# Performance work log

Hardware: AMD Instinct MI355X
Metric: run time of the kernel (lower is better)

Reference implementation:

```python
import jax, jax.numpy as jnp
import numpy as np

E = 1024   # emb_dim
H = 1024   # hidden_size
L = 2      # num_layers
V = 50257  # vocab_size
S = 2048   # encoder input length
T = 2048   # decoder target length


def setup_inputs() -> dict:
    key = jax.random.key(0)
    ks = jax.random.split(key, 16)
    s = 0.02  # init scale
    f32 = jnp.float32
    return {
        "inputs": jax.random.randint(ks[0], (1, S), 0, V),
        "outputs": jax.random.randint(ks[1], (1, T), 0, V),
        "sos": 1,
        "enc_emb": jax.random.normal(ks[2], (V, E), f32) * s,
        "dec_emb": jax.random.normal(ks[3], (V, E), f32) * s,
        # Stacked LSTM weights; layer-0 input dim == E == H so layers stack.
        "enc_Wih": jax.random.normal(ks[4], (L, 4 * H, H), f32) * s,
        "enc_Whh": jax.random.normal(ks[5], (L, 4 * H, H), f32) * s,
        "enc_bih": jax.random.normal(ks[6], (L, 4 * H), f32) * s,
        "enc_bhh": jax.random.normal(ks[7], (L, 4 * H), f32) * s,
        "dec_Wih": jax.random.normal(ks[8], (L, 4 * H, H), f32) * s,
        "dec_Whh": jax.random.normal(ks[9], (L, 4 * H, H), f32) * s,
        "dec_bih": jax.random.normal(ks[10], (L, 4 * H), f32) * s,
        "dec_bhh": jax.random.normal(ks[11], (L, 4 * H), f32) * s,
        "lin_W": jax.random.normal(ks[12], (V, H), f32) * s,
        "lin_b": jax.random.normal(ks[13], (V,), f32) * s,
    }


def _run_stack(xs, Wih, Whh, bih, bhh, h0, c0):
    # xs: [S, E]; Wih/Whh: [L, 4H, H]; h0/c0: [L, H]
    # PyTorch LSTM gate order: i, f, g, o.
    h_fin, c_fin = [], []
    for l in range(Wih.shape[0]):
        Wi, Wh, bi, bh = Wih[l], Whh[l], bih[l], bhh[l]

        def step(carry, x, Wi=Wi, Wh=Wh, bi=bi, bh=bh):
            h, c = carry
            g = Wi @ x + bi + Wh @ h + bh           # [4H]
            i, f, gg, o = jnp.split(g, 4)
            c = jax.nn.sigmoid(f) * c + jax.nn.sigmoid(i) * jnp.tanh(gg)
            h = jax.nn.sigmoid(o) * jnp.tanh(c)
            return (h, c), h

        (h, c), xs = jax.lax.scan(step, (h0[l], c0[l]), xs)
        h_fin.append(h)
        c_fin.append(c)
    return xs, jnp.stack(h_fin), jnp.stack(c_fin)


def reference(inputs, outputs, sos, enc_emb, dec_emb,
              enc_Wih, enc_Whh, enc_bih, enc_bhh,
              dec_Wih, dec_Whh, dec_bih, dec_bhh,
              lin_W, lin_b):
    # Encoder over the source sequence (batch == 1, squeezed away).
    x = enc_emb[inputs[0]]                       # [S, E]
    z = jnp.zeros((L, H), dtype=x.dtype)
    _, hN, cN = _run_stack(x, enc_Wih, enc_Whh, enc_bih, enc_bhh, z, z)
    # Full teacher forcing: decoder inputs are [sos, outputs[:, :-1]].
    dec_tokens = jnp.concatenate(
        [jnp.array([sos], dtype=outputs.dtype), outputs[0, :-1]])
    y = dec_emb[dec_tokens]                      # [T, E]
    dec_out, _, _ = _run_stack(y, dec_Wih, dec_Whh, dec_bih, dec_bhh, hN, cN)
    logits = dec_out @ lin_W.T + lin_b           # [T, V]
    return logits
```

## Files before the change

### kernel.cpp

```cpp
#include <hip/hip_runtime.h>
#include <hip/hip_bf16.h>
#include <math.h>

#define S_LEN 2048
#define T_LEN 2048
#define HID   1024
#define GATES 4096
#define VOCAB 50257

typedef unsigned int u32;
typedef unsigned long long ull;
typedef u32 u32x4 __attribute__((ext_vector_type(4)));

__device__ __forceinline__ float fsig_(float x)  { return 1.0f / (1.0f + __expf(-x)); }
__device__ __forceinline__ float ftanh_(float x) { float e = __expf(2.0f * x); return 1.0f - 2.0f / (e + 1.0f); }

__device__ __forceinline__ u32x4 cload16(const ull* p) {
  u32x4 v;
  asm volatile("global_load_dwordx4 %0, %1, off sc0 sc1\n\ts_waitcnt vmcnt(0)"
               : "=v"(v) : "v"(p) : "memory");
  return v;
}

__global__ void zero_f4(float4* __restrict__ p, size_t n4) {
  size_t i = (size_t)blockIdx.x * blockDim.x + threadIdx.x;
  size_t stride = (size_t)gridDim.x * blockDim.x;
  for (; i < n4; i += stride) p[i] = make_float4(0.f, 0.f, 0.f, 0.f);
}

__global__ void zero_u32(u32* __restrict__ p, int n) {
  int i = blockIdx.x * blockDim.x + threadIdx.x;
  if (i < n) p[i] = 0u;
}

__global__ void build_dec_tokens(const int* __restrict__ outputs, const int* __restrict__ sos,
                                 int* __restrict__ toks, int T) {
  int t = blockIdx.x * blockDim.x + threadIdx.x;
  if (t < T) toks[t] = (t == 0) ? sos[0] : outputs[t - 1];
}

__global__ __launch_bounds__(256) void gemm_xwt(
    const float* __restrict__ X, const float* __restrict__ W,
    const float* __restrict__ b1,
    float* __restrict__ C, int M, int N, int K)
{
  __shared__ float Xs[16][68];
  __shared__ float Ws[16][68];
  const int tid = threadIdx.x;
  const int tx = tid & 15;
  const int ty = tid >> 4;
  const int m0 = blockIdx.y * 64;
  const int n0 = blockIdx.x * 64;
  const int lr = tid >> 2;
  const int lc = (tid & 3) * 4;
  float acc[4][4] = {{0.f}};

  for (int k0 = 0; k0 < K; k0 += 16) {
    float4 xv = *(const float4*)(X + (size_t)(m0 + lr) * K + k0 + lc);
    float4 wv = make_float4(0.f, 0.f, 0.f, 0.f);
    int wr = n0 + lr;
    if (wr < N) wv = *(const float4*)(W + (size_t)wr * K + k0 + lc);
    __syncthreads();
    Xs[lc + 0][lr] = xv.x; Xs[lc + 1][lr] = xv.y; Xs[lc + 2][lr] = xv.z; Xs[lc + 3][lr] = xv.w;
    Ws[lc + 0][lr] = wv.x; Ws[lc + 1][lr] = wv.y; Ws[lc + 2][lr] = wv.z; Ws[lc + 3][lr] = wv.w;
    __syncthreads();
#pragma unroll
    for (int kk = 0; kk < 16; ++kk) {
      float4 a = *(const float4*)&Xs[kk][ty * 4];
      float4 b = *(const float4*)&Ws[kk][tx * 4];
      float av[4] = {a.x, a.y, a.z, a.w};
      float bv[4] = {b.x, b.y, b.z, b.w};
#pragma unroll
      for (int i = 0; i < 4; ++i)
#pragma unroll
        for (int j = 0; j < 4; ++j)
          acc[i][j] = fmaf(av[i], bv[j], acc[i][j]);
    }
  }
#pragma unroll
  for (int i = 0; i < 4; ++i) {
    int m = m0 + ty * 4 + i;
#pragma unroll
    for (int j = 0; j < 4; ++j) {
      int n = n0 + tx * 4 + j;
      if (n < N) C[(size_t)m * N + n] = acc[i][j] + (b1 ? b1[n] : 0.f);
    }
  }
}

__global__ __launch_bounds__(512, 2) void lstm2(
    const float* __restrict__ emb,  const int* __restrict__ toks,
    const float* __restrict__ Wi0,  const float* __restrict__ Wh0,
    const float* __restrict__ bi0,  const float* __restrict__ bh0,
    const float* __restrict__ Wi1,  const float* __restrict__ Wh1,
    const float* __restrict__ bi1,  const float* __restrict__ bh1,
    const float* __restrict__ h00,  const float* __restrict__ c00,
    const float* __restrict__ h01,  const float* __restrict__ c01,
    ull* __restrict__ s0, ull* __restrict__ s1,
    float* __restrict__ hf0, float* __restrict__ cf0,
    float* __restrict__ hf1, float* __restrict__ cf1,
    float* __restrict__ dec_out, int T)
{
  const int tid = threadIdx.x;
  const int wg  = blockIdx.x;
  const bool isL0 = (wg < 128);
  const int wgl = isL0 ? wg : wg - 128;

  const int lane16 = tid & 15;
  const int rloc = tid >> 4;
  const int jloc = rloc & 7;
  const int gate = rloc >> 3;
  const int grow = gate * HID + wgl * 8 + jloc;

  __shared__ float lds_x[2][HID];
  __shared__ float lds_h[HID];
  __shared__ float lds_g[32];
  __shared__ float lds_c[8];

  const float* Wi = isL0 ? Wi0 : Wi1;
  const float* Wh = isL0 ? Wh0 : Wh1;
  const float breg = (isL0 ? (bi0[grow] + bh0[grow]) : (bi1[grow] + bh1[grow]));

  float4 Wir[16], Whr[16];
  {
    const float4* wi = (const float4*)(Wi + (size_t)grow * HID);
    const float4* wh = (const float4*)(Wh + (size_t)grow * HID);
#pragma unroll
    for (int i = 0; i < 16; ++i) {
      Wir[i] = wi[lane16 + i * 16];
      Whr[i] = wh[lane16 + i * 16];
    }
  }

  {
    const float* hini = isL0 ? h00 : h01;
    const float* cini = isL0 ? c00 : c01;
    if (tid < 8) lds_c[tid] = cini[wgl * 8 + tid];
    if (tid < 256) ((float4*)lds_h)[tid] = ((const float4*)hini)[tid];
    if (isL0 && tid < 256) {
      int tok = toks[0];
      ((float4*)lds_x[0])[tid] = ((const float4*)(emb + (size_t)tok * HID))[tid];
    }
  }
  __syncthreads();

  ull* s_mine = isL0 ? s0 : s1;

  for (int t = 0; t < T; ++t) {
    const int cur = t & 1;

    if (isL0) {
      if (t > 0) {
        const ull* ph = s0 + (size_t)(t - 1) * HID + 2 * tid;
        u32x4 v = cload16(ph);
        while (v.y < (u32)t || v.w < (u32)t) v = cload16(ph);
        lds_h[2 * tid]     = __uint_as_float(v.x);
        lds_h[2 * tid + 1] = __uint_as_float(v.z);
      }
    } else {
      const ull* px = s0 + (size_t)t * HID + 2 * tid;
      u32x4 vx = cload16(px);
      while (vx.y < (u32)(t + 1) || vx.w < (u32)(t + 1)) vx = cload16(px);
      lds_x[0][2 * tid]     = __uint_as_float(vx.x);
      lds_x[0][2 * tid + 1] = __uint_as_float(vx.z);
      if (t > 0) {
        const ull* ph = s1 + (size_t)(t - 1) * HID + 2 * tid;
        u32x4 v = cload16(ph);
        while (v.y < (u32)t || v.w < (u32)t) v = cload16(ph);
        lds_h[2 * tid]     = __uint_as_float(v.x);
        lds_h[2 * tid + 1] = __uint_as_float(v.z);
      }
    }
    __syncthreads();

    if (isL0 && tid < 256 && t + 1 < T) {
      int tok = toks[t + 1];
      ((float4*)lds_x[cur ^ 1])[tid] = ((const float4*)(emb + (size_t)tok * HID))[tid];
    }

    const float* xbuf = isL0 ? lds_x[cur] : lds_x[0];
    float p0 = 0.f, p1 = 0.f, p2 = 0.f, p3 = 0.f;
#pragma unroll
    for (int i = 0; i < 16; ++i) {
      const float4 xv = *(const float4*)&xbuf[(lane16 << 2) + (i << 6)];
      p0 = fmaf(Wir[i].x, xv.x, p0);
      p1 = fmaf(Wir[i].y, xv.y, p1);
      p2 = fmaf(Wir[i].z, xv.z, p2);
      p3 = fmaf(Wir[i].w, xv.w, p3);
    }
#pragma unroll
    for (int i = 0; i < 16; ++i) {
      const float4 hv = *(const float4*)&lds_h[(lane16 << 2) + (i << 6)];
      p0 = fmaf(Whr[i].x, hv.x, p0);
      p1 = fmaf(Whr[i].y, hv.y, p1);
      p2 = fmaf(Whr[i].z, hv.z, p2);
      p3 = fmaf(Whr[i].w, hv.w, p3);
    }
    float sum = (p0 + p1) + (p2 + p3);
    sum += __shfl_xor(sum, 1);
    sum += __shfl_xor(sum, 2);
    sum += __shfl_xor(sum, 4);
    sum += __shfl_xor(sum, 8);
    if (lane16 == 0) lds_g[rloc] = sum + breg;
    __syncthreads();

    if (tid < 8) {
      const float gi = lds_g[tid];
      const float gf = lds_g[8 + tid];
      const float gg = lds_g[16 + tid];
      const float go = lds_g[24 + tid];
      const float c = fsig_(gf) * lds_c[tid] + fsig_(gi) * ftanh_(gg);
      const float h = fsig_(go) * ftanh_(c);
      lds_c[tid] = c;
      const int col = wgl * 8 + tid;
      const ull pk = ((ull)(u32)(t + 1) << 32) | (ull)__float_as_uint(h);
      __hip_atomic_store(&s_mine[(size_t)t * HID + col], pk,
                         __ATOMIC_RELAXED, __HIP_MEMORY_SCOPE_AGENT);
      if (!isL0 && dec_out) dec_out[(size_t)t * HID + col] = h;
      if (t == T - 1) {
        if (isL0) { if (hf0) hf0[col] = h; if (cf0) cf0[col] = c; }
        else      { if (hf1) hf1[col] = h; if (cf1) cf1[col] = c; }
      }
    }
  }
}

extern "C" void kernel_launch(void* const* d_in, const int* in_sizes, int n_in,
                              void* d_out, int out_size, void* d_ws, size_t ws_size,
                              hipStream_t stream) {
  const int*   inputs  = (const int*)d_in[0];
  const int*   outputs = (const int*)d_in[1];
  const int*   sos     = (const int*)d_in[2];
  const float* enc_emb = (const float*)d_in[3];
  const float* dec_emb = (const float*)d_in[4];
  const float* enc_Wih = (const float*)d_in[5];
  const float* enc_Whh = (const float*)d_in[6];
  const float* enc_bih = (const float*)d_in[7];
  const float* enc_bhh = (const float*)d_in[8];
  const float* dec_Wih = (const float*)d_in[9];
  const float* dec_Whh = (const float*)d_in[10];
  const float* dec_bih = (const float*)d_in[11];
  const float* dec_bhh = (const float*)d_in[12];
  const float* lin_W   = (const float*)d_in[13];
  const float* lin_b   = (const float*)d_in[14];

  float* out = (float*)d_out;
  ull* s0e = (ull*)d_out;
  ull* s1e = s0e + 2097152;
  ull* s0d = s1e + 2097152;
  ull* s1d = s0d + 2097152;

  char* ws = (char*)d_ws;
  float* zerosv = (float*)(ws + 0);
  float* hf0    = (float*)(ws + 4096);
  float* cf0    = (float*)(ws + 8192);
  float* hf1    = (float*)(ws + 12288);
  float* cf1    = (float*)(ws + 16384);
  int*   dtoks  = (int*)(ws + 20480);
  float* B2     = (float*)(ws + ((size_t)1 << 20));

  const size_t WOFF = (size_t)GATES * HID;

  zero_f4<<<2048, 256, 0, stream>>>((float4*)d_out, 4194304);
  zero_u32<<<4, 256, 0, stream>>>((u32*)zerosv, 1024);
  build_dec_tokens<<<8, 256, 0, stream>>>(outputs, sos, dtoks, T_LEN);

  lstm2<<<256, 512, 0, stream>>>(
      enc_emb, inputs,
      enc_Wih, enc_Whh, enc_bih, enc_bhh,
      enc_Wih + WOFF, enc_Whh + WOFF, enc_bih + GATES, enc_bhh + GATES,
      zerosv, zerosv, zerosv, zerosv,
      s0e, s1e, hf0, cf0, hf1, cf1, nullptr, S_LEN);

  lstm2<<<256, 512, 0, stream>>>(
      dec_emb, dtoks,
      dec_Wih, dec_Whh, dec_bih, dec_bhh,
      dec_Wih + WOFF, dec_Whh + WOFF, dec_bih + GATES, dec_bhh + GATES,
      hf0, cf0, hf1, cf1,
      s0d, s1d, nullptr, nullptr, nullptr, nullptr, B2, T_LEN);

  dim3 gemmV_grid((VOCAB + 63) / 64, T_LEN / 64);
  gemm_xwt<<<gemmV_grid, 256, 0, stream>>>(B2, lin_W, lin_b, out, T_LEN, VOCAB, HID);
}
```

Before: 15.80 ms.

## Relay cross-block hidden-state polling through per-XCD L2 ring buffers

Each XCD elects one block per layer, which polls the device-coherent hidden-state buffer and republishes each step's values into a per-XCD ring buffer stored with L2-only scope. The other blocks on that XCD poll the ring with cheaper L2-scope loads and fall back to device-scope loads only periodically or when they see a newer tag. The goal is to cut the cost of many workgroups spinning on system-coherent loads in the step-serialized LSTM recurrence. It adds an extra hop of latency through the leader and bounded spin caps that could silently accept stale data. It also depends on blocks mapping to XCDs as assumed and on a larger zeroed workspace.

```diff
diff --git a/kernel.cpp b/kernel.cpp
--- a/kernel.cpp
+++ b/kernel.cpp
@@ -7,30 +7,63 @@
 #define HID   1024
 #define GATES 4096
 #define VOCAB 50257
+#define RDEPTH 64
+#define SPINCAP 65536
 
 typedef unsigned int u32;
 typedef unsigned long long ull;
 typedef u32 u32x4 __attribute__((ext_vector_type(4)));
+typedef float f32x4 __attribute__((ext_vector_type(4)));
 
 __device__ __forceinline__ float fsig_(float x)  { return 1.0f / (1.0f + __expf(-x)); }
 __device__ __forceinline__ float ftanh_(float x) { float e = __expf(2.0f * x); return 1.0f - 2.0f / (e + 1.0f); }
 
-__device__ __forceinline__ u32x4 cload16(const ull* p) {
+__device__ __forceinline__ u32x4 cload16_dev(const ull* p) {
   u32x4 v;
   asm volatile("global_load_dwordx4 %0, %1, off sc0 sc1\n\ts_waitcnt vmcnt(0)"
                : "=v"(v) : "v"(p) : "memory");
   return v;
 }
+__device__ __forceinline__ u32x4 cload16_l2(const ull* p) {
+  u32x4 v;
+  asm volatile("global_load_dwordx4 %0, %1, off sc0\n\ts_waitcnt vmcnt(0)"
+               : "=v"(v) : "v"(p) : "memory");
+  return v;
+}
+__device__ __forceinline__ void store16_l2(ull* p, u32x4 v) {
+  asm volatile("global_store_dwordx4 %0, %1, off sc0" :: "v"(p), "v"(v) : "memory");
+}
+
+__device__ __forceinline__ u32x4 poll_ring(const ull* lp, const ull* fp, u32 want) {
+  u32x4 v = cload16_l2(lp);
+  int spins = 0;
+  while (!(v.y == want && v.w == want)) {
+    const bool newer = (v.y > want) || (v.w > want);
+    if (newer || ((++spins & 15) == 0)) {
+      v = cload16_dev(fp);
+      if (v.y == want && v.w == want) break;
+    } else {
+      v = cload16_l2(lp);
+    }
+    if (spins > SPINCAP) break;
+  }
+  return v;
+}
+
+__device__ __forceinline__ u32x4 poll_fab(const ull* fp, u32 want) {
+  u32x4 v = cload16_dev(fp);
+  int spins = 0;
+  while (v.y < want || v.w < want) {
+    if (++spins > SPINCAP) break;
+    v = cload16_dev(fp);
+  }
+  return v;
+}
 
 __global__ void zero_f4(float4* __restrict__ p, size_t n4) {
   size_t i = (size_t)blockIdx.x * blockDim.x + threadIdx.x;
   size_t stride = (size_t)gridDim.x * blockDim.x;
   for (; i < n4; i += stride) p[i] = make_float4(0.f, 0.f, 0.f, 0.f);
-}
-
-__global__ void zero_u32(u32* __restrict__ p, int n) {
-  int i = blockIdx.x * blockDim.x + threadIdx.x;
-  if (i < n) p[i] = 0u;
 }
 
 __global__ void build_dec_tokens(const int* __restrict__ outputs, const int* __restrict__ sos,
@@ -97,6 +130,8 @@
     const float* __restrict__ h00,  const float* __restrict__ c00,
     const float* __restrict__ h01,  const float* __restrict__ c01,
     ull* __restrict__ s0, ull* __restrict__ s1,
+    ull* __restrict__ ring,
+    u32* __restrict__ elect,
     float* __restrict__ hf0, float* __restrict__ cf0,
     float* __restrict__ hf1, float* __restrict__ cf1,
     float* __restrict__ dec_out, int T)
@@ -116,21 +151,39 @@
   __shared__ float lds_h[HID];
   __shared__ float lds_g[32];
   __shared__ float lds_c[8];
+  __shared__ u32 sh_xcd, sh_duty;
+
+  if (tid == 0) {
+    u32 xcc;
+    asm volatile("s_getreg_b32 %0, hwreg(HW_REG_XCC_ID)" : "=s"(xcc));
+    xcc &= 7;
+    u32 duty = 0, exp = 0;
+    if (isL0) {
+      if (__hip_atomic_compare_exchange_strong(&elect[xcc * 2 + 0], &exp, 1u,
+            __ATOMIC_RELAXED, __ATOMIC_RELAXED, __HIP_MEMORY_SCOPE_AGENT)) duty |= 1;
+    } else {
+      if (__hip_atomic_compare_exchange_strong(&elect[xcc * 2 + 1], &exp, 1u,
+            __ATOMIC_RELAXED, __ATOMIC_RELAXED, __HIP_MEMORY_SCOPE_AGENT)) duty |= 2;
+    }
+    sh_xcd = xcc; sh_duty = duty;
+  }
 
   const float* Wi = isL0 ? Wi0 : Wi1;
   const float* Wh = isL0 ? Wh0 : Wh1;
   const float breg = (isL0 ? (bi0[grow] + bh0[grow]) : (bi1[grow] + bh1[grow]));
-
-  float4 Wir[16], Whr[16];
+  f32x4 Wir[16], Whr[16];
   {
-    const float4* wi = (const float4*)(Wi + (size_t)grow * HID);
-    const float4* wh = (const float4*)(Wh + (size_t)grow * HID);
+    const f32x4* wi = (const f32x4*)(Wi + (size_t)grow * HID);
+    const f32x4* wh = (const f32x4*)(Wh + (size_t)grow * HID);
 #pragma unroll
     for (int i = 0; i < 16; ++i) {
       Wir[i] = wi[lane16 + i * 16];
       Whr[i] = wh[lane16 + i * 16];
     }
   }
+#pragma unroll
+  for (int i = 0; i < 16; ++i)
+    asm volatile("" : "+v"(Wir[i]), "+v"(Whr[i]));
 
   {
     const float* hini = isL0 ? h00 : h01;
@@ -143,7 +196,9 @@
     }
   }
   __syncthreads();
-
+  const u32 duty = sh_duty;
+  ull* ring0 = ring + ((size_t)sh_xcd * 2 + 0) * RDEPTH * HID;
+  ull* ring1 = ring + ((size_t)sh_xcd * 2 + 1) * RDEPTH * HID;
   ull* s_mine = isL0 ? s0 : s1;
 
   for (int t = 0; t < T; ++t) {
@@ -151,22 +206,31 @@
 
     if (isL0) {
       if (t > 0) {
-        const ull* ph = s0 + (size_t)(t - 1) * HID + 2 * tid;
-        u32x4 v = cload16(ph);
-        while (v.y < (u32)t || v.w < (u32)t) v = cload16(ph);
+        const int idx = t - 1; const u32 want = (u32)t;
+        const ull* fp = s0 + (size_t)idx * HID + 2 * tid;
+        ull* rp = ring0 + (size_t)(idx & (RDEPTH - 1)) * HID + 2 * tid;
+        u32x4 v;
+        if (duty & 1) { v = poll_fab(fp, want); store16_l2(rp, v); }
+        else          { v = poll_ring(rp, fp, want); }
         lds_h[2 * tid]     = __uint_as_float(v.x);
         lds_h[2 * tid + 1] = __uint_as_float(v.z);
       }
     } else {
-      const ull* px = s0 + (size_t)t * HID + 2 * tid;
-      u32x4 vx = cload16(px);
-      while (vx.y < (u32)(t + 1) || vx.w < (u32)(t + 1)) vx = cload16(px);
-      lds_x[0][2 * tid]     = __uint_as_float(vx.x);
-      lds_x[0][2 * tid + 1] = __uint_as_float(vx.z);
+      {
+        const int idx = t; const u32 want = (u32)(t + 1);
+        const ull* fp = s0 + (size_t)idx * HID + 2 * tid;
+        const ull* rp = ring0 + (size_t)(idx & (RDEPTH - 1)) * HID + 2 * tid;
+        u32x4 v = poll_ring(rp, fp, want);
+        lds_x[0][2 * tid]     = __uint_as_float(v.x);
+        lds_x[0][2 * tid + 1] = __uint_as_float(v.z);
+      }
       if (t > 0) {
-        const ull* ph = s1 + (size_t)(t - 1) * HID + 2 * tid;
-        u32x4 v = cload16(ph);
-        while (v.y < (u32)t || v.w < (u32)t) v = cload16(ph);
+        const int idx = t - 1; const u32 want = (u32)t;
+        const ull* fp = s1 + (size_t)idx * HID + 2 * tid;
+        ull* rp = ring1 + (size_t)(idx & (RDEPTH - 1)) * HID + 2 * tid;
+        u32x4 v;
+        if (duty & 2) { v = poll_fab(fp, want); store16_l2(rp, v); }
+        else          { v = poll_ring(rp, fp, want); }
         lds_h[2 * tid]     = __uint_as_float(v.x);
         lds_h[2 * tid + 1] = __uint_as_float(v.z);
       }
@@ -222,6 +286,13 @@
         else      { if (hf1) hf1[col] = h; if (cf1) cf1[col] = c; }
       }
     }
+  }
+
+  if (isL0 && (duty & 1)) {
+    const int idx = T - 1; const u32 want = (u32)T;
+    const ull* fp = s0 + (size_t)idx * HID + 2 * tid;
+    u32x4 v = poll_fab(fp, want);
+    store16_l2(ring0 + (size_t)(idx & (RDEPTH - 1)) * HID + 2 * tid, v);
   }
 }
 
@@ -251,18 +322,22 @@
   ull* s1d = s0d + 2097152;
 
   char* ws = (char*)d_ws;
-  float* zerosv = (float*)(ws + 0);
-  float* hf0    = (float*)(ws + 4096);
-  float* cf0    = (float*)(ws + 8192);
-  float* hf1    = (float*)(ws + 12288);
-  float* cf1    = (float*)(ws + 16384);
-  int*   dtoks  = (int*)(ws + 20480);
-  float* B2     = (float*)(ws + ((size_t)1 << 20));
+  ull*   ring_e  = (ull*)(ws + 0);
+  ull*   ring_d  = (ull*)(ws + ((size_t)8 << 20));
+  u32*   elect_e = (u32*)(ws + ((size_t)16 << 20));
+  u32*   elect_d = (u32*)(ws + ((size_t)16 << 20) + 128);
+  float* zerosv  = (float*)(ws + ((size_t)16 << 20) + 4096);
+  float* hf0     = (float*)(ws + ((size_t)16 << 20) + 8192);
+  float* cf0     = (float*)(ws + ((size_t)16 << 20) + 12288);
+  float* hf1     = (float*)(ws + ((size_t)16 << 20) + 16384);
+  float* cf1     = (float*)(ws + ((size_t)16 << 20) + 20480);
+  int*   dtoks   = (int*)(ws + ((size_t)16 << 20) + 24576);
+  float* B2      = (float*)(ws + ((size_t)17 << 20));
 
   const size_t WOFF = (size_t)GATES * HID;
 
   zero_f4<<<2048, 256, 0, stream>>>((float4*)d_out, 4194304);
-  zero_u32<<<4, 256, 0, stream>>>((u32*)zerosv, 1024);
+  zero_f4<<<2048, 256, 0, stream>>>((float4*)ws, ((size_t)17 << 20) / 16);
   build_dec_tokens<<<8, 256, 0, stream>>>(outputs, sos, dtoks, T_LEN);
 
   lstm2<<<256, 512, 0, stream>>>(
@@ -270,14 +345,14 @@
       enc_Wih, enc_Whh, enc_bih, enc_bhh,
       enc_Wih + WOFF, enc_Whh + WOFF, enc_bih + GATES, enc_bhh + GATES,
       zerosv, zerosv, zerosv, zerosv,
-      s0e, s1e, hf0, cf0, hf1, cf1, nullptr, S_LEN);
+      s0e, s1e, ring_e, elect_e, hf0, cf0, hf1, cf1, nullptr, S_LEN);
 
   lstm2<<<256, 512, 0, stream>>>(
       dec_emb, dtoks,
       dec_Wih, dec_Whh, dec_bih, dec_bhh,
       dec_Wih + WOFF, dec_Whh + WOFF, dec_bih + GATES, dec_bhh + GATES,
       hf0, cf0, hf1, cf1,
-      s0d, s1d, nullptr, nullptr, nullptr, nullptr, B2, T_LEN);
+      s0d, s1d, ring_d, elect_d, nullptr, nullptr, nullptr, nullptr, B2, T_LEN);
 
   dim3 gemmV_grid((VOCAB + 63) / 64, T_LEN / 64);
   gemm_xwt<<<gemmV_grid, 256, 0, stream>>>(B2, lin_W, lin_b, out, T_LEN, VOCAB, HID);
```

Result: slower. 25.00 ms (+58.3%).
